# Kernel tuning notes

Hardware: AMD Instinct MI355X
Metric: run time of the kernel (lower is better)

The kernel has to match this reference:

```python
import jax, jax.numpy as jnp
import numpy as np

B, S, D = 4, 2048, 1024
E, F = 8, 4096


def setup_inputs() -> dict:
    key = jax.random.key(0)
    ks = jax.random.split(key, 5)
    x = jax.random.normal(ks[0], (B, S, D), dtype=jnp.float32)
    switch_w = jax.random.normal(ks[1], (D, E), dtype=jnp.float32) * (D ** -0.5)
    switch_b = jnp.zeros((E,), dtype=jnp.float32)
    w1 = jax.random.normal(ks[2], (E, D, F), dtype=jnp.float32) * (D ** -0.5)
    b1 = jnp.zeros((E, F), dtype=jnp.float32)
    w2 = jax.random.normal(ks[3], (E, F, D), dtype=jnp.float32) * (F ** -0.5)
    b2 = jnp.zeros((E, D), dtype=jnp.float32)
    return {"x": x, "switch_w": switch_w, "switch_b": switch_b,
            "w1": w1, "b1": b1, "w2": w2, "b2": b2}


def reference(x, switch_w, switch_b, w1, b1, w2, b2):
    b, s, d = x.shape
    t = x.reshape(-1, d)                                  # [T, D] tokens
    logits = t @ switch_w + switch_b                      # [T, E]
    route_prob = jax.nn.softmax(logits, axis=-1)
    route_prob_max = jnp.max(route_prob, axis=-1)         # [T]
    routes = jnp.argmax(route_prob, axis=-1)              # [T] top-1 expert

    out = jnp.zeros_like(t)
    n_experts = w1.shape[0]
    for e in range(n_experts):                            # small fixed expert loop
        h = jax.nn.gelu(t @ w1[e] + b1[e])                # [T, F]
        y = h @ w2[e] + b2[e]                             # [T, D]
        mask = (routes == e)[:, None]
        out = jnp.where(mask, y, out)                     # scatter-combine by route

    out = out * route_prob_max[:, None]                   # is_scale_prob=True
    return out.reshape(b, s, d)
```

## Files before the change

kernel.cpp:

```cpp
#include <hip/hip_runtime.h>
#include <hip/hip_bf16.h>
#include <math.h>

#define T_TOK 8192
#define DIM   1024
#define NEXP  8
#define FF    4096
#define BM    256
#define BN    256
#define BK    64
#define TPAD  (T_TOK + NEXP * BM)
#define NCBLK 32

typedef __attribute__((ext_vector_type(4))) float  f32x4;
typedef __attribute__((ext_vector_type(8))) __bf16 bf16x8;

__global__ __launch_bounds__(256) void router_kernel(const float* __restrict__ x,
                              const float* __restrict__ sw, const float* __restrict__ sb,
                              int* __restrict__ route, float* __restrict__ scale,
                              __hip_bfloat16* __restrict__ xb)
{
    int wave = threadIdx.x >> 6, lane = threadIdx.x & 63;
    int t = blockIdx.x * 4 + wave;
    const float* xr = x + (size_t)t * DIM + lane * 16;

    float xv[16];
#pragma unroll
    for (int i = 0; i < 4; ++i)
        *(float4*)&xv[i * 4] = *(const float4*)(xr + i * 4);

    bf16x8 u0, u1;
#pragma unroll
    for (int i = 0; i < 8; ++i) { u0[i] = (__bf16)xv[i]; u1[i] = (__bf16)xv[i + 8]; }
    __hip_bfloat16* xo = xb + (size_t)t * DIM + lane * 16;
    *(bf16x8*)xo = u0;
    *(bf16x8*)(xo + 8) = u1;

    double acc[NEXP];
#pragma unroll
    for (int e = 0; e < NEXP; ++e) acc[e] = 0.0;
    const float* swp = sw + lane * 16 * NEXP;
#pragma unroll
    for (int j = 0; j < 16; ++j) {
        float4 s0 = *(const float4*)(swp + j * 8);
        float4 s1 = *(const float4*)(swp + j * 8 + 4);
        double xd = (double)xv[j];
        acc[0] += xd * (double)s0.x; acc[1] += xd * (double)s0.y;
        acc[2] += xd * (double)s0.z; acc[3] += xd * (double)s0.w;
        acc[4] += xd * (double)s1.x; acc[5] += xd * (double)s1.y;
        acc[6] += xd * (double)s1.z; acc[7] += xd * (double)s1.w;
    }
#pragma unroll
    for (int e = 0; e < NEXP; ++e) {
        double v = acc[e];
        for (int off = 32; off; off >>= 1) v += __shfl_down(v, off);
        acc[e] = v;
    }
    if (lane == 0) {
        double m = -1e300; int am = 0;
#pragma unroll
        for (int e = 0; e < NEXP; ++e) {
            double v = acc[e] + (double)sb[e];
            acc[e] = v;
            if (v > m) { m = v; am = e; }
        }
        double s = 0.0;
#pragma unroll
        for (int e = 0; e < NEXP; ++e) s += exp(acc[e] - m);
        route[t] = am;
        scale[t] = (float)(1.0 / s);
    }
}

__global__ __launch_bounds__(256) void count_kernel(const int* __restrict__ route,
                                                    int* __restrict__ bc)
{
    __shared__ int c[NEXP];
    if (threadIdx.x < NEXP) c[threadIdx.x] = 0;
    __syncthreads();
    int t = blockIdx.x * 256 + threadIdx.x;
    atomicAdd(&c[route[t]], 1);
    __syncthreads();
    if (threadIdx.x < NEXP) bc[blockIdx.x * NEXP + threadIdx.x] = c[threadIdx.x];
}

__global__ __launch_bounds__(64) void offsets_kernel(const int* __restrict__ bc,
                                                     int* __restrict__ offPad,
                                                     int* __restrict__ base)
{
    int l = threadIdx.x & 31;
    int cnt[NEXP], pre[NEXP], tot[NEXP];
#pragma unroll
    for (int e = 0; e < NEXP; ++e) cnt[e] = bc[l * NEXP + e];
#pragma unroll
    for (int e = 0; e < NEXP; ++e) {
        int v = cnt[e];
#pragma unroll
        for (int d = 1; d < 32; d <<= 1) {
            int u = __shfl_up(v, d, 32);
            if (l >= d) v += u;
        }
        pre[e] = v - cnt[e];
        tot[e] = __shfl(v, 31, 32);
    }
    int o = 0, off[NEXP];
#pragma unroll
    for (int e = 0; e < NEXP; ++e) {
        off[e] = o;
        o += ((tot[e] + BM - 1) / BM) * BM;
    }
    if (l == 0) {
#pragma unroll
        for (int e = 0; e < NEXP; ++e) offPad[e] = off[e];
        offPad[NEXP] = o;
    }
#pragma unroll
    for (int e = 0; e < NEXP; ++e) base[l * NEXP + e] = off[e] + pre[e];
}

__global__ __launch_bounds__(256) void scatter_kernel(const int* __restrict__ route,
                                                      const int* __restrict__ base,
                                                      int* __restrict__ perm)
{
    __shared__ int cur[NEXP];
    if (threadIdx.x < NEXP) cur[threadIdx.x] = base[blockIdx.x * NEXP + threadIdx.x];
    __syncthreads();
    int t = blockIdx.x * 256 + threadIdx.x;
    int pos = atomicAdd(&cur[route[t]], 1);
    perm[pos] = t;
}

__global__ __launch_bounds__(256) void transpose_cvt64(const float* __restrict__ src,
                                                       __hip_bfloat16* __restrict__ dst,
                                                       int R, int C)
{
    __shared__ float tile[64][65];
    size_t bofs = (size_t)blockIdx.z * (size_t)R * (size_t)C;
    int c0 = blockIdx.x * 64, r0 = blockIdx.y * 64;
    int t = threadIdx.x;
    int tx = t & 15, ty = t >> 4;
#pragma unroll
    for (int i = 0; i < 4; ++i) {
        int r = ty + i * 16;
        float4 v = *(const float4*)(src + bofs + (size_t)(r0 + r) * C + c0 + tx * 4);
        tile[r][tx * 4 + 0] = v.x; tile[r][tx * 4 + 1] = v.y;
        tile[r][tx * 4 + 2] = v.z; tile[r][tx * 4 + 3] = v.w;
    }
    __syncthreads();
    int sx = t & 7, sy = t >> 3;
#pragma unroll
    for (int i = 0; i < 2; ++i) {
        int oc = sy + i * 32;
        bf16x8 u;
#pragma unroll
        for (int j = 0; j < 8; ++j)
            u[j] = (__bf16)tile[sx * 8 + j][oc];
        *(bf16x8*)(dst + bofs + (size_t)(c0 + oc) * R + r0 + sx * 8) = u;
    }
}

#define STAGE_A(b, h, t) do { \
    __builtin_amdgcn_global_load_lds((const __attribute__((address_space(1))) void*)(aSrc[h][0] + (size_t)(t) * 64), \
        (__attribute__((address_space(3))) void*)(ldsA + (b) * 32768 + (h) * 16384 + wid * 1024), 16, 0, 0); \
    __builtin_amdgcn_global_load_lds((const __attribute__((address_space(1))) void*)(aSrc[h][1] + (size_t)(t) * 64), \
        (__attribute__((address_space(3))) void*)(ldsA + (b) * 32768 + (h) * 16384 + (wid + 8) * 1024), 16, 0, 0); \
} while (0)

#define STAGE_B(b, h, t) do { \
    __builtin_amdgcn_global_load_lds((const __attribute__((address_space(1))) void*)(bSrc[h][0] + (size_t)(t) * 64), \
        (__attribute__((address_space(3))) void*)(ldsB + (b) * 32768 + (h) * 16384 + wid * 1024), 16, 0, 0); \
    __builtin_amdgcn_global_load_lds((const __attribute__((address_space(1))) void*)(bSrc[h][1] + (size_t)(t) * 64), \
        (__attribute__((address_space(3))) void*)(ldsB + (b) * 32768 + (h) * 16384 + (wid + 8) * 1024), 16, 0, 0); \
} while (0)

#define VMW asm volatile("s_waitcnt vmcnt(4)" ::: "memory")

#define PHASE(B_, MH, KS, LOADB, STAGEX, VMX) do { \
    __builtin_amdgcn_sched_barrier(0); \
    bf16x8 af[4]; \
    _Pragma("unroll") \
    for (int i_ = 0; i_ < 4; ++i_) \
        af[i_] = *(const bf16x8*)(aRd + (B_) * 32768 + ((MH) * 4 + i_) * 2048 + kOff[KS]); \
    if (LOADB) { \
        _Pragma("unroll") \
        for (int n_ = 0; n_ < 4; ++n_) \
            bfr[KS][n_] = *(const bf16x8*)(bRd + (B_) * 32768 + n_ * 2048 + kOff[KS]); \
    } \
    STAGEX; \
    __builtin_amdgcn_s_barrier(); \
    asm volatile("s_waitcnt lgkmcnt(0)" ::: "memory"); \
    __builtin_amdgcn_sched_barrier(0); \
    __builtin_amdgcn_s_setprio(1); \
    _Pragma("unroll") \
    for (int i_ = 0; i_ < 4; ++i_) \
        _Pragma("unroll") \
        for (int n_ = 0; n_ < 4; ++n_) \
            acc[(MH) * 4 + i_][n_] = __builtin_amdgcn_mfma_f32_16x16x32_bf16(af[i_], bfr[KS][n_], acc[(MH) * 4 + i_][n_], 0, 0, 0); \
    __builtin_amdgcn_s_setprio(0); \
    VMX; \
    __builtin_amdgcn_s_barrier(); \
} while (0)

template<int MODE>
__global__ __launch_bounds__(512, 2) void moe_gemm8(
    const __hip_bfloat16* __restrict__ A,
    const __hip_bfloat16* __restrict__ Bw,
    const float* __restrict__ bias,
    const int* __restrict__ offPad,
    const int* __restrict__ perm,
    const float* __restrict__ scale,
    __hip_bfloat16* __restrict__ Hout,
    float* __restrict__ Out,
    const int K, const int N)
{
    const int nwg = gridDim.x * gridDim.y;
    const int bid = blockIdx.y * gridDim.x + blockIdx.x;
    const int swz = (bid & 7) * (nwg >> 3) + (bid >> 3);
    const int nt = swz % gridDim.x;
    const int mt = swz / gridDim.x;
    const int m0 = mt * BM;
    if (m0 >= offPad[NEXP]) return;
    int e = 0;
    while (offPad[e + 1] <= m0) ++e;

    __shared__ char lds[131072];
    char* ldsA = lds;
    char* ldsB = lds + 65536;

    const int tid  = threadIdx.x;
    const int lane = tid & 63;
    const int wid  = tid >> 6;
    const int wr   = wid >> 2;
    const int wc   = wid & 3;
    const int g    = lane >> 4, rl = lane & 15;

    const __hip_bfloat16* Bp = Bw + (size_t)e * (size_t)N * (size_t)K;

    const int l3 = lane >> 3;
    const int colOff = ((lane & 7) ^ l3) * 8;
    const __hip_bfloat16* aSrc[2][2];
    const __hip_bfloat16* bSrc[2][2];
#pragma unroll
    for (int h = 0; h < 2; ++h)
#pragma unroll
        for (int j = 0; j < 2; ++j) {
            int r = (wid + j * 8) * 8 + l3;
            int arow = m0 + h * 128 + r;
            size_t ar;
            if (MODE == 0) { int tk = perm[arow]; ar = (size_t)(tk < 0 ? 0 : tk); }
            else           { ar = (size_t)arow; }
            aSrc[h][j] = A + ar * (size_t)K + colOff;
            bSrc[h][j] = Bp + (size_t)(nt * BN + h * 128 + r) * (size_t)K + colOff;
        }

    const char* aRd = ldsA + wr * 16384 + rl * 128;
    const char* bRd = ldsB + (wc >> 1) * 16384 + (wc & 1) * 8192 + rl * 128;
    int kOff[2];
    kOff[0] = ((0 * 4 + g) ^ (rl & 7)) * 16;
    kOff[1] = ((1 * 4 + g) ^ (rl & 7)) * 16;

    f32x4 acc[8][4];
#pragma unroll
    for (int i = 0; i < 8; ++i)
#pragma unroll
        for (int n = 0; n < 4; ++n) acc[i][n] = (f32x4)0.0f;
    bf16x8 bfr[2][4];

    const int ntiles = K >> 6;

    STAGE_A(0, 0, 0); STAGE_A(0, 1, 0);
    STAGE_B(0, 0, 0); STAGE_B(0, 1, 0);
    {
        int t1p = 1 < ntiles ? 1 : ntiles - 1;
        STAGE_B(1, 0, t1p); STAGE_B(1, 1, t1p);
    }
    asm volatile("s_waitcnt vmcnt(4)" ::: "memory");
    __builtin_amdgcn_s_barrier();

    for (int it = 0; it < (ntiles >> 1); ++it) {
        const int t1 = 2 * it + 1;
        const int t2 = 2 * it + 2 < ntiles ? 2 * it + 2 : ntiles - 1;
        const int t3 = 2 * it + 3 < ntiles ? 2 * it + 3 : ntiles - 1;
        PHASE(0, 0, 0, true,  STAGE_A(1, 0, t1), );
        PHASE(0, 0, 1, true,  STAGE_A(1, 1, t1), );
        PHASE(0, 1, 0, false, STAGE_B(0, 0, t2), );
        PHASE(0, 1, 1, false, STAGE_B(0, 1, t2), VMW);
        PHASE(1, 0, 0, true,  STAGE_A(0, 0, t2), );
        PHASE(1, 0, 1, true,  STAGE_A(0, 1, t2), );
        PHASE(1, 1, 0, false, STAGE_B(1, 0, t3), );
        PHASE(1, 1, 1, false, STAGE_B(1, 1, t3), VMW);
    }
    asm volatile("s_waitcnt vmcnt(0)" ::: "memory");

    const int colBase = nt * BN + wc * 64;
    const int rowBase = m0 + wr * 128;
    float bcol[4];
#pragma unroll
    for (int n = 0; n < 4; ++n) bcol[n] = bias[(size_t)e * N + colBase + n * 16 + rl];

    if (MODE == 0) {
#pragma unroll
        for (int m = 0; m < 8; ++m) {
#pragma unroll
            for (int r = 0; r < 4; ++r) {
                int row = rowBase + m * 16 + g * 4 + r;
                __hip_bfloat16* hrow = Hout + (size_t)row * N + colBase;
#pragma unroll
                for (int n = 0; n < 4; ++n) {
                    float v = acc[m][n][r] + bcol[n];
                    float u = -1.5957691216057308f * (v + 0.044715f * v * v * v);
                    float gel = v / (1.f + __expf(u));
                    hrow[n * 16 + rl] = __float2bfloat16(gel);
                }
            }
        }
    } else {
#pragma unroll
        for (int m = 0; m < 8; ++m) {
#pragma unroll
            for (int r = 0; r < 4; ++r) {
                int row = rowBase + m * 16 + g * 4 + r;
                int tk = perm[row];
                if (tk >= 0) {
                    float sc = scale[tk];
                    float* orow = Out + (size_t)tk * N + colBase;
#pragma unroll
                    for (int n = 0; n < 4; ++n)
                        orow[n * 16 + rl] = (acc[m][n][r] + bcol[n]) * sc;
                }
            }
        }
    }
}

extern "C" void kernel_launch(void* const* d_in, const int* in_sizes, int n_in,
                              void* d_out, int out_size, void* d_ws, size_t ws_size,
                              hipStream_t stream)
{
    const float* x  = (const float*)d_in[0];
    const float* sw = (const float*)d_in[1];
    const float* sb = (const float*)d_in[2];
    const float* w1 = (const float*)d_in[3];
    const float* b1 = (const float*)d_in[4];
    const float* w2 = (const float*)d_in[5];
    const float* b2 = (const float*)d_in[6];
    float* out = (float*)d_out;
    char* ws = (char*)d_ws;

    int*   bc     = (int*)(ws + 0);
    int*   base   = (int*)(ws + 1024);
    int*   offPad = (int*)(ws + 2048);
    int*   route  = (int*)(ws + 4096);
    float* scale  = (float*)(ws + 36864);
    int*   perm   = (int*)(ws + 69632);
    __hip_bfloat16* xb  = (__hip_bfloat16*)(ws + 131072);
    __hip_bfloat16* w1t = (__hip_bfloat16*)(ws + 16908288);
    __hip_bfloat16* w2t = (__hip_bfloat16*)(ws + 16908288);
    __hip_bfloat16* h   = (__hip_bfloat16*)(ws + 84017152);

    hipMemsetAsync(perm, 0xFF, TPAD * 4, stream);

    router_kernel<<<T_TOK / 4, 256, 0, stream>>>(x, sw, sb, route, scale, xb);
    count_kernel<<<NCBLK, 256, 0, stream>>>(route, bc);
    offsets_kernel<<<1, 64, 0, stream>>>(bc, offPad, base);
    scatter_kernel<<<NCBLK, 256, 0, stream>>>(route, base, perm);

    transpose_cvt64<<<dim3(FF / 64, DIM / 64, NEXP), 256, 0, stream>>>(w1, w1t, DIM, FF);

    moe_gemm8<0><<<dim3(FF / BN, TPAD / BM), 512, 0, stream>>>(
        xb, w1t, b1, offPad, perm, scale, h, nullptr, DIM, FF);

    transpose_cvt64<<<dim3(DIM / 64, FF / 64, NEXP), 256, 0, stream>>>(w2, w2t, FF, DIM);

    moe_gemm8<1><<<dim3(DIM / BN, TPAD / BM), 512, 0, stream>>>(
        h, w2t, b2, offPad, perm, scale, nullptr, out, FF, DIM);
}
```

Baseline: 336.8 us.

## Fuse both expert GEMMs into one persistent ticketed kernel with split-K second GEMM

Merges the two grouped GEMMs into one launch. Blocks take work items in order from an atomic ticket counter, and second-GEMM tiles spin on a per-row-block completion counter until all 16 first-GEMM tiles for that row block are done. This lets the second GEMM start on finished rows while the first GEMM is still running, removing the tail and launch gap between the stages. It also moves the w2 transpose ahead of the first GEMM and, when the workspace is large enough, splits K of the second GEMM in two, writing one half into a partial buffer that a separate reduce kernel adds back. The cost is spin-waiting blocks that occupy CUs, an extra partial write and read pass for the split-K, and a dependence on workspace size for which path runs.

```diff
diff --git a/kernel.cpp b/kernel.cpp
--- a/kernel.cpp
+++ b/kernel.cpp
@@ -11,6 +11,7 @@
 #define BK    64
 #define TPAD  (T_TOK + NEXP * BM)
 #define NCBLK 32
+#define NG1   640
 
 typedef __attribute__((ext_vector_type(4))) float  f32x4;
 typedef __attribute__((ext_vector_type(8))) __bf16 bf16x8;
@@ -157,6 +158,16 @@
             u[j] = (__bf16)tile[sx * 8 + j][oc];
         *(bf16x8*)(dst + bofs + (size_t)(c0 + oc) * R + r0 + sx * 8) = u;
     }
+}
+
+__global__ __launch_bounds__(256) void reduce_kernel(float* __restrict__ out,
+                                                     const float* __restrict__ part1)
+{
+    size_t i = ((size_t)blockIdx.x * 256 + threadIdx.x) * 4;
+    float4 a = *(const float4*)(out + i);
+    float4 b = *(const float4*)(part1 + i);
+    a.x += b.x; a.y += b.y; a.z += b.z; a.w += b.w;
+    *(float4*)(out + i) = a;
 }
 
 #define STAGE_A(b, h, t) do { \
@@ -201,27 +212,54 @@
     __builtin_amdgcn_s_barrier(); \
 } while (0)
 
-template<int MODE>
-__global__ __launch_bounds__(512, 2) void moe_gemm8(
-    const __hip_bfloat16* __restrict__ A,
-    const __hip_bfloat16* __restrict__ Bw,
-    const float* __restrict__ bias,
+__global__ __launch_bounds__(512, 2) void moe_work(
+    const __hip_bfloat16* __restrict__ xb,
+    const __hip_bfloat16* __restrict__ w1t,
+    const float* __restrict__ b1,
+    const __hip_bfloat16* __restrict__ w2t,
+    const float* __restrict__ b2,
+    __hip_bfloat16* __restrict__ hbuf,
+    float* __restrict__ out,
+    float* __restrict__ part1,
     const int* __restrict__ offPad,
     const int* __restrict__ perm,
     const float* __restrict__ scale,
-    __hip_bfloat16* __restrict__ Hout,
-    float* __restrict__ Out,
-    const int K, const int N)
-{
-    const int nwg = gridDim.x * gridDim.y;
-    const int bid = blockIdx.y * gridDim.x + blockIdx.x;
-    const int swz = (bid & 7) * (nwg >> 3) + (bid >> 3);
-    const int nt = swz % gridDim.x;
-    const int mt = swz / gridDim.x;
+    int* __restrict__ tickets,
+    int* __restrict__ done1,
+    const int itemBase, const int slot, const int kSplit)
+{
+    __shared__ int sItem;
+    if (threadIdx.x == 0) sItem = itemBase + atomicAdd(&tickets[slot], 1);
+    __syncthreads();
+    const int item = sItem;
+
+    int MODE, nt, mt, kz;
+    const int ks = kSplit - 1;
+    if (item < NG1) { MODE = 0; nt = item & 15; mt = item >> 4; kz = 0; }
+    else {
+        int j = item - NG1; MODE = 1;
+        kz = j & ks;
+        nt = (j >> ks) & 3;
+        mt = j >> (2 + ks);
+    }
     const int m0 = mt * BM;
     if (m0 >= offPad[NEXP]) return;
+
+    const int K = MODE ? FF : DIM;
+    const int N = MODE ? DIM : FF;
+    const int kwidth = MODE ? (K >> ks) : K;
+    const int kbase  = MODE ? kz * kwidth : 0;
+    const __hip_bfloat16* A  = MODE ? hbuf : xb;
+    const __hip_bfloat16* Bw = MODE ? w2t : w1t;
+    const float* bias = MODE ? b2 : b1;
+
     int e = 0;
     while (offPad[e + 1] <= m0) ++e;
+
+    if (MODE) {
+        while (__hip_atomic_load(&done1[mt], __ATOMIC_ACQUIRE, __HIP_MEMORY_SCOPE_AGENT) < 16)
+            __builtin_amdgcn_s_sleep(2);
+    }
 
     __shared__ char lds[131072];
     char* ldsA = lds;
@@ -247,10 +285,10 @@
             int r = (wid + j * 8) * 8 + l3;
             int arow = m0 + h * 128 + r;
             size_t ar;
-            if (MODE == 0) { int tk = perm[arow]; ar = (size_t)(tk < 0 ? 0 : tk); }
-            else           { ar = (size_t)arow; }
-            aSrc[h][j] = A + ar * (size_t)K + colOff;
-            bSrc[h][j] = Bp + (size_t)(nt * BN + h * 128 + r) * (size_t)K + colOff;
+            if (!MODE) { int tk = perm[arow]; ar = (size_t)(tk < 0 ? 0 : tk); }
+            else       { ar = (size_t)arow; }
+            aSrc[h][j] = A + ar * (size_t)K + kbase + colOff;
+            bSrc[h][j] = Bp + (size_t)(nt * BN + h * 128 + r) * (size_t)K + kbase + colOff;
         }
 
     const char* aRd = ldsA + wr * 16384 + rl * 128;
@@ -266,14 +304,11 @@
         for (int n = 0; n < 4; ++n) acc[i][n] = (f32x4)0.0f;
     bf16x8 bfr[2][4];
 
-    const int ntiles = K >> 6;
+    const int ntiles = kwidth >> 6;
 
     STAGE_A(0, 0, 0); STAGE_A(0, 1, 0);
     STAGE_B(0, 0, 0); STAGE_B(0, 1, 0);
-    {
-        int t1p = 1 < ntiles ? 1 : ntiles - 1;
-        STAGE_B(1, 0, t1p); STAGE_B(1, 1, t1p);
-    }
+    STAGE_B(1, 0, 1); STAGE_B(1, 1, 1);
     asm volatile("s_waitcnt vmcnt(4)" ::: "memory");
     __builtin_amdgcn_s_barrier();
 
@@ -296,15 +331,16 @@
     const int rowBase = m0 + wr * 128;
     float bcol[4];
 #pragma unroll
-    for (int n = 0; n < 4; ++n) bcol[n] = bias[(size_t)e * N + colBase + n * 16 + rl];
-
-    if (MODE == 0) {
+    for (int n = 0; n < 4; ++n)
+        bcol[n] = (!MODE || kz == 0) ? bias[(size_t)e * N + colBase + n * 16 + rl] : 0.f;
+
+    if (!MODE) {
 #pragma unroll
         for (int m = 0; m < 8; ++m) {
 #pragma unroll
             for (int r = 0; r < 4; ++r) {
                 int row = rowBase + m * 16 + g * 4 + r;
-                __hip_bfloat16* hrow = Hout + (size_t)row * N + colBase;
+                __hip_bfloat16* hrow = hbuf + (size_t)row * N + colBase;
 #pragma unroll
                 for (int n = 0; n < 4; ++n) {
                     float v = acc[m][n][r] + bcol[n];
@@ -314,7 +350,12 @@
                 }
             }
         }
+        __threadfence();
+        __syncthreads();
+        if (threadIdx.x == 0)
+            __hip_atomic_fetch_add(&done1[mt], 1, __ATOMIC_RELEASE, __HIP_MEMORY_SCOPE_AGENT);
     } else {
+        float* O = kz ? part1 : out;
 #pragma unroll
         for (int m = 0; m < 8; ++m) {
 #pragma unroll
@@ -323,7 +364,7 @@
                 int tk = perm[row];
                 if (tk >= 0) {
                     float sc = scale[tk];
-                    float* orow = Out + (size_t)tk * N + colBase;
+                    float* orow = O + (size_t)tk * N + colBase;
 #pragma unroll
                     for (int n = 0; n < 4; ++n)
                         orow[n * 16 + rl] = (acc[m][n][r] + bcol[n]) * sc;
@@ -347,17 +388,37 @@
     float* out = (float*)d_out;
     char* ws = (char*)d_ws;
 
-    int*   bc     = (int*)(ws + 0);
-    int*   base   = (int*)(ws + 1024);
-    int*   offPad = (int*)(ws + 2048);
-    int*   route  = (int*)(ws + 4096);
-    float* scale  = (float*)(ws + 36864);
-    int*   perm   = (int*)(ws + 69632);
-    __hip_bfloat16* xb  = (__hip_bfloat16*)(ws + 131072);
-    __hip_bfloat16* w1t = (__hip_bfloat16*)(ws + 16908288);
-    __hip_bfloat16* w2t = (__hip_bfloat16*)(ws + 16908288);
-    __hip_bfloat16* h   = (__hip_bfloat16*)(ws + 84017152);
-
+    int*   tickets = (int*)(ws + 0);
+    int*   done1   = (int*)(ws + 64);
+    int*   bc      = (int*)(ws + 1024);
+    int*   base    = (int*)(ws + 2048);
+    int*   offPad  = (int*)(ws + 3072);
+    int*   route   = (int*)(ws + 4096);
+    float* scale   = (float*)(ws + 36864);
+    int*   perm    = (int*)(ws + 69632);
+
+    const size_t offXb = 131072;
+    const size_t szXb  = (size_t)T_TOK * DIM * 2;
+    const size_t offW1 = offXb + szXb;
+    const size_t szW   = (size_t)NEXP * DIM * FF * 2;
+    const size_t offW2A = offW1 + szW;
+    const size_t szH   = (size_t)TPAD * FF * 2;
+    const size_t offHA = offW2A + szW;
+    const size_t offP1 = offHA + szH;
+    const size_t needA = offP1 + (size_t)T_TOK * DIM * 4;
+    const size_t needB = offP1;
+
+    const bool tierA = ws_size >= needA;
+    const bool tierB = !tierA && ws_size >= needB;
+    const bool fused = tierA || tierB;
+
+    __hip_bfloat16* xb  = (__hip_bfloat16*)(ws + offXb);
+    __hip_bfloat16* w1t = (__hip_bfloat16*)(ws + offW1);
+    __hip_bfloat16* w2t = (__hip_bfloat16*)(ws + (fused ? offW2A : offW1));
+    __hip_bfloat16* h   = (__hip_bfloat16*)(ws + (fused ? offHA : offW2A));
+    float*          p1  = (float*)(ws + offP1);
+
+    hipMemsetAsync(ws, 0, 4096, stream);
     hipMemsetAsync(perm, 0xFF, TPAD * 4, stream);
 
     router_kernel<<<T_TOK / 4, 256, 0, stream>>>(x, sw, sb, route, scale, xb);
@@ -367,11 +428,22 @@
 
     transpose_cvt64<<<dim3(FF / 64, DIM / 64, NEXP), 256, 0, stream>>>(w1, w1t, DIM, FF);
 
-    moe_gemm8<0><<<dim3(FF / BN, TPAD / BM), 512, 0, stream>>>(
-        xb, w1t, b1, offPad, perm, scale, h, nullptr, DIM, FF);
-
-    transpose_cvt64<<<dim3(DIM / 64, FF / 64, NEXP), 256, 0, stream>>>(w2, w2t, FF, DIM);
-
-    moe_gemm8<1><<<dim3(DIM / BN, TPAD / BM), 512, 0, stream>>>(
-        h, w2t, b2, offPad, perm, scale, nullptr, out, FF, DIM);
-}
+    if (fused) {
+        transpose_cvt64<<<dim3(DIM / 64, FF / 64, NEXP), 256, 0, stream>>>(w2, w2t, FF, DIM);
+        const int kSplit = tierA ? 2 : 1;
+        const int nItems = NG1 + 160 * kSplit;
+        moe_work<<<nItems, 512, 0, stream>>>(xb, w1t, b1, w2t, b2, h, out, p1,
+                                             offPad, perm, scale, tickets, done1,
+                                             0, 0, kSplit);
+        if (tierA)
+            reduce_kernel<<<(T_TOK * DIM) / 1024, 256, 0, stream>>>(out, p1);
+    } else {
+        moe_work<<<NG1, 512, 0, stream>>>(xb, w1t, b1, w2t, b2, h, out, p1,
+                                          offPad, perm, scale, tickets, done1,
+                                          0, 0, 1);
+        transpose_cvt64<<<dim3(DIM / 64, FF / 64, NEXP), 256, 0, stream>>>(w2, w2t, FF, DIM);
+        moe_work<<<160, 512, 0, stream>>>(xb, w1t, b1, w2t, b2, h, out, p1,
+                                          offPad, perm, scale, tickets, done1,
+                                          NG1, 1, 1);
+    }
+}
```

Measured after the change: 583.2 us. +73.2%, slower.

## Fuse w2 transpose-convert into first expert GEMM launch as extra blocks

Applied to the files above, without the earlier changes.

When the workspace is large enough, the w2 fp32-to-bf16 transpose is done by extra workgroups appended to the first expert GEMM grid, giving w2t its own buffer so it no longer aliases w1t. This removes one kernel launch and lets the transpose overlap with the GEMM tail instead of running serially between the two GEMMs. The GEMM grid also becomes 1D with swizzle ordering changed to iterate M tiles fastest within an N column, which alters cache reuse. It needs more workspace and falls back to the old sequence if that space is unavailable.

```diff
diff --git a/kernel.cpp b/kernel.cpp
--- a/kernel.cpp
+++ b/kernel.cpp
@@ -11,6 +11,10 @@
 #define BK    64
 #define TPAD  (T_TOK + NEXP * BM)
 #define NCBLK 32
+#define MT    (TPAD / BM)
+#define NG1   640
+#define NG2   160
+#define NT2   4096
 
 typedef __attribute__((ext_vector_type(4))) float  f32x4;
 typedef __attribute__((ext_vector_type(8))) __bf16 bf16x8;
@@ -211,23 +215,60 @@
     const float* __restrict__ scale,
     __hip_bfloat16* __restrict__ Hout,
     float* __restrict__ Out,
+    const float* __restrict__ w2src,
+    __hip_bfloat16* __restrict__ w2tdst,
     const int K, const int N)
 {
-    const int nwg = gridDim.x * gridDim.y;
-    const int bid = blockIdx.y * gridDim.x + blockIdx.x;
-    const int swz = (bid & 7) * (nwg >> 3) + (bid >> 3);
-    const int nt = swz % gridDim.x;
-    const int mt = swz / gridDim.x;
-    const int m0 = mt * BM;
+    __shared__ char lds[131072];
+    const int tid = threadIdx.x;
+    const int bid = blockIdx.x;
+    const int NG  = MODE ? NG2 : NG1;
+
+    if (MODE == 0 && bid >= NG1) {
+        const int j    = bid - NG1;
+        const int t2   = tid & 255;
+        const int half = tid >> 8;
+        const int tile_id = j * 2 + half;
+        const int cx = tile_id & 15;
+        const int ry = (tile_id >> 4) & 63;
+        const int ez = tile_id >> 10;
+        float (*tl)[65] = (float (*)[65])(lds + half * 17408);
+        const float* src = w2src + (size_t)ez * FF * DIM;
+        __hip_bfloat16* dst = w2tdst + (size_t)ez * DIM * FF;
+        const int c0 = cx * 64, r0 = ry * 64;
+        const int tx = t2 & 15, ty = t2 >> 4;
+#pragma unroll
+        for (int i = 0; i < 4; ++i) {
+            int r = ty + i * 16;
+            float4 v = *(const float4*)(src + (size_t)(r0 + r) * DIM + c0 + tx * 4);
+            tl[r][tx * 4 + 0] = v.x; tl[r][tx * 4 + 1] = v.y;
+            tl[r][tx * 4 + 2] = v.z; tl[r][tx * 4 + 3] = v.w;
+        }
+        __syncthreads();
+        const int sx = t2 & 7, sy = t2 >> 3;
+#pragma unroll
+        for (int i = 0; i < 2; ++i) {
+            int oc = sy + i * 32;
+            bf16x8 u;
+#pragma unroll
+            for (int jj = 0; jj < 8; ++jj)
+                u[jj] = (__bf16)tl[sx * 8 + jj][oc];
+            *(bf16x8*)(dst + (size_t)(c0 + oc) * FF + r0 + sx * 8) = u;
+        }
+        return;
+    }
+
+    const int swz = (bid & 7) * (NG >> 3) + (bid >> 3);
+    const int mt  = swz % MT;
+    const int nt  = swz / MT;
+    const int m0  = mt * BM;
     if (m0 >= offPad[NEXP]) return;
     int e = 0;
     while (offPad[e + 1] <= m0) ++e;
 
-    __shared__ char lds[131072];
     char* ldsA = lds;
     char* ldsB = lds + 65536;
 
-    const int tid  = threadIdx.x;
     const int lane = tid & 63;
     const int wid  = tid >> 6;
     const int wr   = wid >> 2;
@@ -270,10 +311,7 @@
 
     STAGE_A(0, 0, 0); STAGE_A(0, 1, 0);
     STAGE_B(0, 0, 0); STAGE_B(0, 1, 0);
-    {
-        int t1p = 1 < ntiles ? 1 : ntiles - 1;
-        STAGE_B(1, 0, t1p); STAGE_B(1, 1, t1p);
-    }
+    STAGE_B(1, 0, 1); STAGE_B(1, 1, 1);
     asm volatile("s_waitcnt vmcnt(4)" ::: "memory");
     __builtin_amdgcn_s_barrier();
 
@@ -347,16 +385,28 @@
     float* out = (float*)d_out;
     char* ws = (char*)d_ws;
 
-    int*   bc     = (int*)(ws + 0);
-    int*   base   = (int*)(ws + 1024);
-    int*   offPad = (int*)(ws + 2048);
+    int*   bc     = (int*)(ws + 1024);
+    int*   base   = (int*)(ws + 2048);
+    int*   offPad = (int*)(ws + 3072);
     int*   route  = (int*)(ws + 4096);
     float* scale  = (float*)(ws + 36864);
     int*   perm   = (int*)(ws + 69632);
-    __hip_bfloat16* xb  = (__hip_bfloat16*)(ws + 131072);
-    __hip_bfloat16* w1t = (__hip_bfloat16*)(ws + 16908288);
-    __hip_bfloat16* w2t = (__hip_bfloat16*)(ws + 16908288);
-    __hip_bfloat16* h   = (__hip_bfloat16*)(ws + 84017152);
+
+    const size_t offXb   = 131072;
+    const size_t szXb    = (size_t)T_TOK * DIM * 2;
+    const size_t offW1   = offXb + szXb;
+    const size_t szW     = (size_t)NEXP * DIM * FF * 2;
+    const size_t offW2   = offW1 + szW;
+    const size_t szH     = (size_t)TPAD * FF * 2;
+    const size_t offHF   = offW2 + szW;
+    const size_t needF   = offHF + szH;
+
+    const bool fuseT = ws_size >= needF;
+
+    __hip_bfloat16* xb  = (__hip_bfloat16*)(ws + offXb);
+    __hip_bfloat16* w1t = (__hip_bfloat16*)(ws + offW1);
+    __hip_bfloat16* w2t = (__hip_bfloat16*)(ws + (fuseT ? offW2 : offW1));
+    __hip_bfloat16* h   = (__hip_bfloat16*)(ws + (fuseT ? offHF : offW2));
 
     hipMemsetAsync(perm, 0xFF, TPAD * 4, stream);
 
@@ -367,11 +417,16 @@
 
     transpose_cvt64<<<dim3(FF / 64, DIM / 64, NEXP), 256, 0, stream>>>(w1, w1t, DIM, FF);
 
-    moe_gemm8<0><<<dim3(FF / BN, TPAD / BM), 512, 0, stream>>>(
-        xb, w1t, b1, offPad, perm, scale, h, nullptr, DIM, FF);
-
-    transpose_cvt64<<<dim3(DIM / 64, FF / 64, NEXP), 256, 0, stream>>>(w2, w2t, FF, DIM);
-
-    moe_gemm8<1><<<dim3(DIM / BN, TPAD / BM), 512, 0, stream>>>(
-        h, w2t, b2, offPad, perm, scale, nullptr, out, FF, DIM);
-}
+    if (fuseT) {
+        moe_gemm8<0><<<NG1 + NT2, 512, 0, stream>>>(
+            xb, w1t, b1, offPad, perm, scale, h, nullptr, w2, w2t, DIM, FF);
+        moe_gemm8<1><<<NG2, 512, 0, stream>>>(
+            h, w2t, b2, offPad, perm, scale, nullptr, out, nullptr, nullptr, FF, DIM);
+    } else {
+        moe_gemm8<0><<<NG1, 512, 0, stream>>>(
+            xb, w1t, b1, offPad, perm, scale, h, nullptr, nullptr, nullptr, DIM, FF);
+        transpose_cvt64<<<dim3(DIM / 64, FF / 64, NEXP), 256, 0, stream>>>(w2, w2t, FF, DIM);
+        moe_gemm8<1><<<NG2, 512, 0, stream>>>(
+            h, w2t, b2, offPad, perm, scale, nullptr, out, nullptr, nullptr, FF, DIM);
+    }
+}
```

After: 315.6 us. 1.07x faster.
